# Optimization experiments

Hardware: AMD Instinct MI355X
Metric: run time of the kernel (lower is better)

The kernel has to match this reference:

```python
import jax, jax.numpy as jnp
import numpy as np

N_HEADS = 16


def setup_inputs() -> dict:
    key = jax.random.key(0)
    k0, k1, k2 = jax.random.split(key, 3)
    B, S, D = 8, 1024, 1024
    x = jax.random.normal(k0, (B, S, D), dtype=jnp.float32)
    W_qkv = jax.random.normal(k1, (D, 3 * D), dtype=jnp.float32) * 0.02
    b_qkv = jnp.zeros((3 * D,), dtype=jnp.float32)
    W_proj = jax.random.normal(k2, (D, D), dtype=jnp.float32) * 0.02
    b_proj = jnp.zeros((D,), dtype=jnp.float32)
    return {"x": x, "W_qkv": W_qkv, "b_qkv": b_qkv, "W_proj": W_proj, "b_proj": b_proj}


def reference(x, W_qkv, b_qkv, W_proj, b_proj):
    B, S, D = x.shape
    H = N_HEADS
    hd = D // H
    scale = hd ** (-0.5)
    # qkv projection: (B,S,3D) -> (3,B,H,S,hd)
    qkv = x @ W_qkv + b_qkv
    qkv = qkv.reshape(B, S, 3, H, hd).transpose(2, 0, 3, 1, 4)
    q, k, v = qkv[0], qkv[1], qkv[2]
    # explicit materialized attention scores (B,H,S,S), softmax over keys
    scores = jnp.einsum("bhqd,bhkd->bhqk", q, k) * scale
    attn = jax.nn.softmax(scores, axis=-1)
    # weighted values -> concat heads -> output projection
    out = jnp.einsum("bhqk,bhkd->bhqd", attn, v)
    out = out.transpose(0, 2, 1, 3).reshape(B, S, D)
    return out @ W_proj + b_proj
```

## Files before the change

### kernel.cpp

```cpp
#include <hip/hip_runtime.h>
#include <hip/hip_bf16.h>

typedef __bf16 bf16_t;
typedef __attribute__((ext_vector_type(8))) __bf16 bf16x8;
typedef __attribute__((ext_vector_type(4))) float f32x4;
typedef __attribute__((ext_vector_type(16))) float f32x16;

#define QSCALE 0.18033688011112042f
#define RESCALE_THR 11.5f

#define OFF_XB      ((size_t)0)
#define OFF_WQKVT   ((size_t)16777216)
#define OFF_WPROJT  ((size_t)(16777216 + 6291456))
#define OFF_Q       ((size_t)(16777216 + 6291456 + 2097152))
#define OFF_K       (OFF_Q + (size_t)16777216)
#define OFF_V       (OFF_K + (size_t)16777216)
#define OFF_O       OFF_XB

typedef const __attribute__((address_space(1))) void* as1cv;
typedef __attribute__((address_space(3))) void* as3v;

__device__ __forceinline__ void load_lds16(const void* g, void* l) {
  __builtin_amdgcn_global_load_lds((as1cv)g, (as3v)l, 16, 0, 0);
}

__device__ __forceinline__ f32x4 mfma16(bf16x8 a, bf16x8 b, f32x4 c) {
  return __builtin_amdgcn_mfma_f32_16x16x32_bf16(a, b, c, 0, 0, 0);
}
__device__ __forceinline__ f32x16 mfma32(bf16x8 a, bf16x8 b, f32x16 c) {
  return __builtin_amdgcn_mfma_f32_32x32x16_bf16(a, b, c, 0, 0, 0);
}

__device__ __forceinline__ float fexp2(float x) { return __builtin_amdgcn_exp2f(x); }

__device__ __forceinline__ unsigned pack2bf(float a, float b) {
  union { bf16_t h[2]; unsigned u; } x;
  x.h[0] = (bf16_t)a; x.h[1] = (bf16_t)b;
  return x.u;
}

__device__ __forceinline__ bf16x8 frag_from_words(unsigned w0, unsigned w1,
                                                  unsigned w2, unsigned w3) {
  union { unsigned u[4]; bf16x8 v; } x;
  x.u[0] = w0; x.u[1] = w1; x.u[2] = w2; x.u[3] = w3;
  return x.v;
}

__device__ __forceinline__ bf16x8 ldsr(const bf16_t* lds, int row, int slotbyte) {
  return *(const bf16x8*)((const char*)lds + row * 128 +
                          (slotbyte ^ ((row & 7) << 4)));
}


__global__ __launch_bounds__(256) void cvt_bf16_kernel(
    const float* __restrict__ in, bf16_t* __restrict__ out, int n8) {
  int i = blockIdx.x * blockDim.x + threadIdx.x;
  if (i >= n8) return;
  const float4* p = (const float4*)in + (size_t)i * 2;
  float4 a = p[0], b = p[1];
  bf16x8 o;
  o[0] = (bf16_t)a.x; o[1] = (bf16_t)a.y; o[2] = (bf16_t)a.z; o[3] = (bf16_t)a.w;
  o[4] = (bf16_t)b.x; o[5] = (bf16_t)b.y; o[6] = (bf16_t)b.z; o[7] = (bf16_t)b.w;
  ((bf16x8*)out)[i] = o;
}

__global__ __launch_bounds__(256) void transpose_cvt(
    const float* __restrict__ W, bf16_t* __restrict__ Wt, int rows, int cols) {
  __shared__ float t[32][33];
  const int c0 = blockIdx.x * 32, r0 = blockIdx.y * 32;
  const int tx = threadIdx.x, ty = threadIdx.y;
  for (int rr = ty; rr < 32; rr += 8)
    t[rr][tx] = W[(size_t)(r0 + rr) * cols + c0 + tx];
  __syncthreads();
  for (int rr = ty; rr < 32; rr += 8)
    Wt[(size_t)(c0 + rr) * rows + r0 + tx] = (bf16_t)t[tx][rr];
}


__device__ __forceinline__ void gemm_mainloop_1024(
    const bf16_t* __restrict__ A, const bf16_t* __restrict__ Bt,
    int m0, int n0, bf16_t* Alds, bf16_t* Blds, f32x4 acc[4][4]) {
  const int tid = threadIdx.x;
  const int w = tid >> 6, lane = tid & 63;
  const int wr = w >> 1, wc = w & 1;
  const int lr = lane & 15, lg = lane >> 4;
#pragma unroll
  for (int m = 0; m < 4; ++m)
#pragma unroll
    for (int n = 0; n < 4; ++n)
      acc[m][n] = f32x4{0.f, 0.f, 0.f, 0.f};

  const int crow = lane >> 3;
  const int cels = (((lane & 7) ^ crow) * 8);
  const int rx = (lr & 7) << 4;

  for (int kt = 0; kt < 16; ++kt) {
    const int k0 = kt * 64;
#pragma unroll
    for (int it = 0; it < 4; ++it) {
      const int c = it * 4 + w;
      const int rA = c * 8 + crow;
      load_lds16(A + (size_t)(m0 + rA) * 1024 + k0 + cels, (char*)Alds + c * 1024);
      load_lds16(Bt + (size_t)(n0 + rA) * 1024 + k0 + cels, (char*)Blds + c * 1024);
    }
    asm volatile("s_waitcnt vmcnt(0)" ::: "memory");
    __syncthreads();

    bf16x8 af[4][2], bfr[4][2];
#pragma unroll
    for (int m = 0; m < 4; ++m)
#pragma unroll
      for (int kk = 0; kk < 2; ++kk)
        af[m][kk] = *(const bf16x8*)((const char*)Alds + (wr * 64 + m * 16 + lr) * 128 +
                                     ((kk * 64 + lg * 16) ^ rx));
#pragma unroll
    for (int n = 0; n < 4; ++n)
#pragma unroll
      for (int kk = 0; kk < 2; ++kk)
        bfr[n][kk] = *(const bf16x8*)((const char*)Blds + (wc * 64 + n * 16 + lr) * 128 +
                                      ((kk * 64 + lg * 16) ^ rx));
#pragma unroll
    for (int kk = 0; kk < 2; ++kk)
#pragma unroll
      for (int m = 0; m < 4; ++m)
#pragma unroll
        for (int n = 0; n < 4; ++n)
          acc[m][n] = mfma16(af[m][kk], bfr[n][kk], acc[m][n]);
    __syncthreads();
  }
}


__global__ __launch_bounds__(256) void gemm_qkv(
    const bf16_t* __restrict__ A, const bf16_t* __restrict__ Bt,
    const float* __restrict__ bias,
    bf16_t* __restrict__ Qh, bf16_t* __restrict__ Kh, bf16_t* __restrict__ Vt) {
  __shared__ alignas(128) bf16_t Alds[128 * 64];
  __shared__ alignas(128) bf16_t Blds[128 * 64];
  const int m0 = blockIdx.x * 128, n0 = blockIdx.y * 128;
  f32x4 acc[4][4];
  gemm_mainloop_1024(A, Bt, m0, n0, Alds, Blds, acc);

  const int tid = threadIdx.x, w = tid >> 6, lane = tid & 63;
  const int wr = w >> 1, wc = w & 1, lr = lane & 15, lg = lane >> 4;
  const int section = n0 >> 10;
#pragma unroll
  for (int n = 0; n < 4; ++n) {
    const int c = n0 + wc * 64 + n * 16 + lr;
    const float bi = bias[c];
    const int d1024 = c & 1023;
    const int h = d1024 >> 6, d = d1024 & 63;
#pragma unroll
    for (int m = 0; m < 4; ++m) {
#pragma unroll
      for (int j = 0; j < 4; ++j) {
        const int r = m0 + wr * 64 + m * 16 + lg * 4 + j;
        const int b = r >> 10, s = r & 1023;
        const size_t hb = ((size_t)(b * 16 + h)) << 16;
        const float v = acc[m][n][j] + bi;
        if (section == 0)      Qh[hb + (size_t)s * 64 + d] = (bf16_t)(v * QSCALE);
        else if (section == 1) Kh[hb + (size_t)s * 64 + d] = (bf16_t)v;
        else                   Vt[hb + (size_t)d * 1024 + s] = (bf16_t)v;
      }
    }
  }
}


__global__ __launch_bounds__(256) void gemm_out(
    const bf16_t* __restrict__ A, const bf16_t* __restrict__ Bt,
    const float* __restrict__ bias, float* __restrict__ out) {
  __shared__ alignas(128) bf16_t Alds[128 * 64];
  __shared__ alignas(128) bf16_t Blds[128 * 64];
  const int m0 = blockIdx.x * 128, n0 = blockIdx.y * 128;
  f32x4 acc[4][4];
  gemm_mainloop_1024(A, Bt, m0, n0, Alds, Blds, acc);

  const int tid = threadIdx.x, w = tid >> 6, lane = tid & 63;
  const int wr = w >> 1, wc = w & 1, lr = lane & 15, lg = lane >> 4;
#pragma unroll
  for (int n = 0; n < 4; ++n) {
    const int c = n0 + wc * 64 + n * 16 + lr;
    const float bi = bias[c];
#pragma unroll
    for (int m = 0; m < 4; ++m)
#pragma unroll
      for (int j = 0; j < 4; ++j) {
        const int r = m0 + wr * 64 + m * 16 + lg * 4 + j;
        out[(size_t)r * 1024 + c] = acc[m][n][j] + bi;
      }
  }
}


__global__ __launch_bounds__(256, 4) void attn_kernel(
    const bf16_t* __restrict__ Qh, const bf16_t* __restrict__ Kh,
    const bf16_t* __restrict__ Vt, bf16_t* __restrict__ Ob) {
  __shared__ alignas(128) bf16_t Klds[2][64 * 64];
  __shared__ alignas(128) bf16_t Vlds[2][64 * 64];

  const int x = blockIdx.x;
  const int bh = ((x & 7) << 4) | (x >> 6);
  const int qt = (x >> 3) & 7;
  const int b = bh >> 4, h = bh & 15;
  const int tid = threadIdx.x, w = tid >> 6, lane = tid & 63;
  const int q31 = lane & 31, hi = lane >> 5;
  const size_t base = (size_t)bh << 16;

  const int qrow0 = qt * 128 + w * 32;

  bf16x8 qf[4];
#pragma unroll
  for (int c = 0; c < 4; ++c)
    qf[c] = *(const bf16x8*)(Qh + base + (size_t)(qrow0 + q31) * 64 + hi * 8 + 16 * c);

  f32x16 oacc0, oacc1;
#pragma unroll
  for (int r = 0; r < 16; ++r) { oacc0[r] = 0.f; oacc1[r] = 0.f; }
  float mreg = -1e30f, lreg = 0.f;

  const int srow = lane >> 3;
  const int sslot = (((lane & 7) ^ srow) << 3);

#define STAGE_KV(bsel, kt_)                                                        \
  do {                                                                             \
    _Pragma("unroll")                                                              \
    for (int it = 0; it < 2; ++it) {                                               \
      const int c = it * 4 + w;                                                    \
      const int r = c * 8 + srow;                                                  \
      load_lds16(Kh + base + (size_t)((kt_) * 64 + r) * 64 + sslot,                \
                 (char*)&Klds[bsel][0] + c * 1024);                                \
      load_lds16(Vt + base + (size_t)r * 1024 + (kt_) * 64 + sslot,                \
                 (char*)&Vlds[bsel][0] + c * 1024);                                \
    }                                                                              \
  } while (0)

  STAGE_KV(0, 0);
  asm volatile("s_waitcnt vmcnt(0)" ::: "memory");
  __syncthreads();
  int cur = 0;

  for (int kt = 0; kt < 16; ++kt) {
    if (kt + 1 < 16) STAGE_KV(cur ^ 1, kt + 1);

    const bf16_t* Kb = &Klds[cur][0];
    const bf16_t* Vb = &Vlds[cur][0];

    f32x16 st0, st1;
#pragma unroll
    for (int r = 0; r < 16; ++r) { st0[r] = 0.f; st1[r] = 0.f; }
#pragma unroll
    for (int c = 0; c < 4; ++c) {
      const int sb = hi * 16 + 32 * c;
      bf16x8 k0 = ldsr(Kb, q31, sb);
      bf16x8 k1 = ldsr(Kb, 32 + q31, sb);
      __builtin_amdgcn_s_setprio(1);
      st0 = mfma32(k0, qf[c], st0);
      st1 = mfma32(k1, qf[c], st1);
      __builtin_amdgcn_s_setprio(0);
    }

    float mx[8];
#pragma unroll
    for (int r = 0; r < 8; ++r)
      mx[r] = fmaxf(fmaxf(st0[r], st0[r + 8]), fmaxf(st1[r], st1[r + 8]));
#pragma unroll
    for (int r = 0; r < 4; ++r) mx[r] = fmaxf(mx[r], mx[r + 4]);
    float tm = fmaxf(fmaxf(mx[0], mx[1]), fmaxf(mx[2], mx[3]));
    tm = fmaxf(tm, __shfl_xor(tm, 32));

    if (!__all(tm - mreg <= RESCALE_THR)) {
      const float mnew = fmaxf(mreg, tm);
      const float corr = fexp2(mreg - mnew);
      lreg *= corr;
#pragma unroll
      for (int r = 0; r < 16; ++r) { oacc0[r] *= corr; oacc1[r] *= corr; }
      mreg = mnew;
    }

    bf16x8 pa[4];
    float psum = 0.f;
#define GROUP(KC, STV, BASE)                                                   \
    {                                                                          \
      const float e0 = fexp2(STV[BASE + 0] - mreg);                            \
      const float e1 = fexp2(STV[BASE + 1] - mreg);                            \
      const float e2 = fexp2(STV[BASE + 2] - mreg);                            \
      const float e3 = fexp2(STV[BASE + 3] - mreg);                            \
      const float e4 = fexp2(STV[BASE + 4] - mreg);                            \
      const float e5 = fexp2(STV[BASE + 5] - mreg);                            \
      const float e6 = fexp2(STV[BASE + 6] - mreg);                            \
      const float e7 = fexp2(STV[BASE + 7] - mreg);                            \
      psum += ((e0 + e1) + (e2 + e3)) + ((e4 + e5) + (e6 + e7));               \
      unsigned wa = pack2bf(e0, e1), wb = pack2bf(e4, e5);                     \
      asm volatile("v_permlane32_swap_b32 %0, %1" : "+v"(wa), "+v"(wb));       \
      unsigned wc = pack2bf(e2, e3), wd = pack2bf(e6, e7);                     \
      asm volatile("v_permlane32_swap_b32 %0, %1" : "+v"(wc), "+v"(wd));       \
      pa[KC] = frag_from_words(wa, wc, wb, wd);                                \
    }
    GROUP(0, st0, 0)
    GROUP(1, st0, 8)
    GROUP(2, st1, 0)
    GROUP(3, st1, 8)
#undef GROUP
    lreg += psum + __shfl_xor(psum, 32);

#pragma unroll
    for (int kc = 0; kc < 4; ++kc) {
      const int sb = hi * 16 + 32 * kc;
      bf16x8 v0 = ldsr(Vb, q31, sb);
      bf16x8 v1 = ldsr(Vb, 32 + q31, sb);
      __builtin_amdgcn_s_setprio(1);
      oacc0 = mfma32(v0, pa[kc], oacc0);
      oacc1 = mfma32(v1, pa[kc], oacc1);
      __builtin_amdgcn_s_setprio(0);
    }

    asm volatile("s_waitcnt vmcnt(0)" ::: "memory");
    __syncthreads();
    cur ^= 1;
  }
#undef STAGE_KV

  const float inv = 1.0f / lreg;
  const int s_tok = qrow0 + q31;
  bf16_t* obase = Ob + (size_t)(b * 1024 + s_tok) * 1024 + h * 64;
#pragma unroll
  for (int i = 0; i < 8; ++i) {
    const int dbase = ((2 * i) & 3) + 8 * ((2 * i) >> 2) + 4 * hi;
    *(unsigned*)(obase + dbase) =
        pack2bf(oacc0[2 * i] * inv, oacc0[2 * i + 1] * inv);
    *(unsigned*)(obase + 32 + dbase) =
        pack2bf(oacc1[2 * i] * inv, oacc1[2 * i + 1] * inv);
  }
}


extern "C" void kernel_launch(void* const* d_in, const int* in_sizes, int n_in,
                              void* d_out, int out_size, void* d_ws, size_t ws_size,
                              hipStream_t stream) {
  const float* x     = (const float*)d_in[0];
  const float* Wqkv  = (const float*)d_in[1];
  const float* bqkv  = (const float*)d_in[2];
  const float* Wproj = (const float*)d_in[3];
  const float* bproj = (const float*)d_in[4];
  float* out = (float*)d_out;
  char* ws = (char*)d_ws;

  bf16_t* Xb  = (bf16_t*)(ws + OFF_XB);
  bf16_t* Wqt = (bf16_t*)(ws + OFF_WQKVT);
  bf16_t* Wpt = (bf16_t*)(ws + OFF_WPROJT);
  bf16_t* Qh  = (bf16_t*)(ws + OFF_Q);
  bf16_t* Kh  = (bf16_t*)(ws + OFF_K);
  bf16_t* Vt  = (bf16_t*)(ws + OFF_V);
  bf16_t* Ob  = (bf16_t*)(ws + OFF_O);

  cvt_bf16_kernel<<<4096, 256, 0, stream>>>(x, Xb, 1048576);
  transpose_cvt<<<dim3(96, 32), dim3(32, 8), 0, stream>>>(Wqkv, Wqt, 1024, 3072);
  transpose_cvt<<<dim3(32, 32), dim3(32, 8), 0, stream>>>(Wproj, Wpt, 1024, 1024);
  gemm_qkv<<<dim3(64, 24), 256, 0, stream>>>(Xb, Wqt, bqkv, Qh, Kh, Vt);
  attn_kernel<<<1024, 256, 0, stream>>>(Qh, Kh, Vt, Ob);
  gemm_out<<<dim3(64, 8), 256, 0, stream>>>(Ob, Wpt, bproj, out);
}
```

Measured before the change: 179.0 us.

## Double-buffer LDS tiles in GEMM mainloop to overlap loads with MFMA

```diff
diff --git a/kernel.cpp b/kernel.cpp
--- a/kernel.cpp
+++ b/kernel.cpp
@@ -94,40 +94,58 @@
   const int cels = (((lane & 7) ^ crow) * 8);
   const int rx = (lr & 7) << 4;
 
+#define STAGE_AB(bsel, kt_)                                                        \
+  do {                                                                             \
+    _Pragma("unroll")                                                              \
+    for (int it = 0; it < 4; ++it) {                                               \
+      const int c = it * 4 + w;                 \
+      const int rA = c * 8 + crow;                            \
+      load_lds16(A + (size_t)(m0 + rA) * 1024 + (kt_) * 64 + cels,                 \
+                 (char*)Alds + (bsel) * 16384 + c * 1024);                         \
+      load_lds16(Bt + (size_t)(n0 + rA) * 1024 + (kt_) * 64 + cels,                \
+                 (char*)Blds + (bsel) * 16384 + c * 1024);                         \
+    }                                                                              \
+  } while (0)
+
+  STAGE_AB(0, 0);
+  asm volatile("s_waitcnt vmcnt(0)" ::: "memory");
+  __syncthreads();
+  int cur = 0;
+
   for (int kt = 0; kt < 16; ++kt) {
-    const int k0 = kt * 64;
-#pragma unroll
-    for (int it = 0; it < 4; ++it) {
-      const int c = it * 4 + w;
-      const int rA = c * 8 + crow;
-      load_lds16(A + (size_t)(m0 + rA) * 1024 + k0 + cels, (char*)Alds + c * 1024);
-      load_lds16(Bt + (size_t)(n0 + rA) * 1024 + k0 + cels, (char*)Blds + c * 1024);
-    }
+    if (kt + 1 < 16) STAGE_AB(cur ^ 1, kt + 1);
+
+    const char* Ab = (const char*)Alds + cur * 16384;
+    const char* Bb = (const char*)Blds + cur * 16384;
+
+    bf16x8 af[4][2], bfr[4][2];
+#pragma unroll
+    for (int m = 0; m < 4; ++m)
+#pragma unroll
+      for (int kk = 0; kk < 2; ++kk)
+        af[m][kk] = *(const bf16x8*)(Ab + (wr * 64 + m * 16 + lr) * 128 +
+                                     ((kk * 64 + lg * 16) ^ rx));
+#pragma unroll
+    for (int n = 0; n < 4; ++n)
+#pragma unroll
+      for (int kk = 0; kk < 2; ++kk)
+        bfr[n][kk] = *(const bf16x8*)(Bb + (wc * 64 + n * 16 + lr) * 128 +
+                                      ((kk * 64 + lg * 16) ^ rx));
+    __builtin_amdgcn_s_setprio(1);
+#pragma unroll
+    for (int kk = 0; kk < 2; ++kk)
+#pragma unroll
+      for (int m = 0; m < 4; ++m)
+#pragma unroll
+        for (int n = 0; n < 4; ++n)
+          acc[m][n] = mfma16(af[m][kk], bfr[n][kk], acc[m][n]);
+    __builtin_amdgcn_s_setprio(0);
+
     asm volatile("s_waitcnt vmcnt(0)" ::: "memory");
     __syncthreads();
-
-    bf16x8 af[4][2], bfr[4][2];
-#pragma unroll
-    for (int m = 0; m < 4; ++m)
-#pragma unroll
-      for (int kk = 0; kk < 2; ++kk)
-        af[m][kk] = *(const bf16x8*)((const char*)Alds + (wr * 64 + m * 16 + lr) * 128 +
-                                     ((kk * 64 + lg * 16) ^ rx));
-#pragma unroll
-    for (int n = 0; n < 4; ++n)
-#pragma unroll
-      for (int kk = 0; kk < 2; ++kk)
-        bfr[n][kk] = *(const bf16x8*)((const char*)Blds + (wc * 64 + n * 16 + lr) * 128 +
-                                      ((kk * 64 + lg * 16) ^ rx));
-#pragma unroll
-    for (int kk = 0; kk < 2; ++kk)
-#pragma unroll
-      for (int m = 0; m < 4; ++m)
-#pragma unroll
-        for (int n = 0; n < 4; ++n)
-          acc[m][n] = mfma16(af[m][kk], bfr[n][kk], acc[m][n]);
-    __syncthreads();
-  }
+    cur ^= 1;
+  }
+#undef STAGE_AB
 }
 
 
@@ -135,8 +153,8 @@
     const bf16_t* __restrict__ A, const bf16_t* __restrict__ Bt,
     const float* __restrict__ bias,
     bf16_t* __restrict__ Qh, bf16_t* __restrict__ Kh, bf16_t* __restrict__ Vt) {
-  __shared__ alignas(128) bf16_t Alds[128 * 64];
-  __shared__ alignas(128) bf16_t Blds[128 * 64];
+  __shared__ alignas(128) bf16_t Alds[2 * 128 * 64];
+  __shared__ alignas(128) bf16_t Blds[2 * 128 * 64];
   const int m0 = blockIdx.x * 128, n0 = blockIdx.y * 128;
   f32x4 acc[4][4];
   gemm_mainloop_1024(A, Bt, m0, n0, Alds, Blds, acc);
@@ -170,8 +188,8 @@
 __global__ __launch_bounds__(256) void gemm_out(
     const bf16_t* __restrict__ A, const bf16_t* __restrict__ Bt,
     const float* __restrict__ bias, float* __restrict__ out) {
-  __shared__ alignas(128) bf16_t Alds[128 * 64];
-  __shared__ alignas(128) bf16_t Blds[128 * 64];
+  __shared__ alignas(128) bf16_t Alds[2 * 128 * 64];
+  __shared__ alignas(128) bf16_t Blds[2 * 128 * 64];
   const int m0 = blockIdx.x * 128, n0 = blockIdx.y * 128;
   f32x4 acc[4][4];
   gemm_mainloop_1024(A, Bt, m0, n0, Alds, Blds, acc);
```

New measurement: 183.7 us. +2.6%, slower.
